# Kernel tuning notes

Hardware: AMD Instinct MI355X
Metric: run time of the kernel (lower is better)

The kernel has to match this reference:

```python
import jax, jax.numpy as jnp
import numpy as np

GRID_SIZE = 5
SPLINE_ORDER = 3
# Extended knot grid over [-1, 1]: grid_size + 2*spline_order + 1 = 12 knots
_H = 2.0 / GRID_SIZE
GRID = (jnp.arange(-SPLINE_ORDER, GRID_SIZE + SPLINE_ORDER + 1, dtype=jnp.float32) * _H - 1.0)


def b_splines(x):
    # x: [N, F] -> bases [N, F, GRID_SIZE + SPLINE_ORDER]
    g = GRID.astype(x.dtype)
    xe = x[..., None]
    bases = ((xe >= g[:-1]) & (xe < g[1:])).astype(x.dtype)
    for k in range(1, SPLINE_ORDER + 1):
        left = (xe - g[: -(k + 1)]) / (g[k:-1] - g[: -(k + 1)]) * bases[..., :-1]
        right = (g[k + 1:] - xe) / (g[k + 1:] - g[1:-k]) * bases[..., 1:]
        bases = left + right
    return bases


def kan_conv(x, base_w, spline_w, spline_scaler):
    # x: [B, Cin, H, W]; 3x3 conv, stride 1, pad 1 -> [B, Cout, H, W]
    B, C, H, W = x.shape
    patches = jax.lax.conv_general_dilated_patches(
        x, (3, 3), (1, 1), [(1, 1), (1, 1)])  # [B, C*9, H, W]
    feat = patches.transpose(0, 2, 3, 1).reshape(B * H * W, C * 9)
    base_out = jax.nn.silu(feat) @ base_w.T  # [N, Cout]
    bas = b_splines(feat)                    # [N, C*9, 8]
    sw = spline_w * spline_scaler[..., None] # standalone spline scale
    spline_out = jnp.einsum('nik,oik->no', bas, sw)
    out = (base_out + spline_out).reshape(B, H, W, -1).transpose(0, 3, 1, 2)
    return out


def upsample2x(x):
    return jnp.repeat(jnp.repeat(x, 2, axis=2), 2, axis=3)


def setup_inputs() -> dict:
    key = jax.random.key(0)
    ks = jax.random.split(key, 16)
    d = {}
    d['x'] = jax.random.normal(ks[0], (64, 100), dtype=jnp.float32)
    d['lin_w'] = jax.random.normal(ks[1], (2048, 100), dtype=jnp.float32) * 0.1
    d['lin_b'] = jax.random.normal(ks[2], (2048,), dtype=jnp.float32) * 0.01
    chans = [(512, 256), (256, 128), (128, 64), (64, 3)]
    i = 3
    for li, (cin, cout) in enumerate(chans, start=1):
        fin = cin * 9
        scale = 1.0 / np.sqrt(fin)
        d[f'bw{li}'] = jax.random.normal(ks[i], (cout, fin), dtype=jnp.float32) * scale; i += 1
        d[f'sw{li}'] = jax.random.normal(ks[i], (cout, fin, GRID_SIZE + SPLINE_ORDER), dtype=jnp.float32) * (0.1 * scale); i += 1
        d[f'ss{li}'] = jax.random.normal(ks[i], (cout, fin), dtype=jnp.float32) * scale + 1.0; i += 1
    return d


def reference(x, lin_w, lin_b, bw1, sw1, ss1, bw2, sw2, ss2, bw3, sw3, ss3, bw4, sw4, ss4):
    h = jax.nn.relu(x @ lin_w.T + lin_b)          # [B, 2048]
    h = h.reshape(-1, 512, 2, 2)                  # Unflatten
    h = upsample2x(h)                             # 4x4
    h = kan_conv(h, bw1, sw1, ss1)                # [B,256,4,4]
    h = upsample2x(h)                             # 8x8
    h = kan_conv(h, bw2, sw2, ss2)                # [B,128,8,8]
    h = upsample2x(h)                             # 16x16
    h = kan_conv(h, bw3, sw3, ss3)                # [B,64,16,16]
    h = upsample2x(h)                             # 32x32
    h = kan_conv(h, bw4, sw4, ss4)                # [B,3,32,32]
    return jnp.tanh(h)
```

## Files before the change

kernel.cpp:

```cpp
#include <hip/hip_runtime.h>
#include <cstdint>
#include <cmath>

#define BATCH 64

typedef __attribute__((ext_vector_type(8))) __bf16 bf16x8;
typedef __attribute__((ext_vector_type(16))) float f32x16;

__device__ __forceinline__ void expand9(float x, float* e) {
  float t = __expf(-x);
  e[0] = __fdividef(x, 1.f + t);
  float b[11];
#pragma unroll
  for (int j = 0; j < 11; ++j) {
    float gj  = 0.4f * (float)j - 2.2f;
    float gj1 = 0.4f * (float)(j + 1) - 2.2f;
    b[j] = (x >= gj && x < gj1) ? 1.f : 0.f;
  }
#pragma unroll
  for (int k = 1; k <= 3; ++k) {
    float inv = 1.f / (0.4f * (float)k);
#pragma unroll
    for (int j = 0; j < 11 - k; ++j) {
      float gj   = 0.4f * (float)j - 2.2f;
      float gjk1 = 0.4f * (float)(j + k + 1) - 2.2f;
      b[j] = ((x - gj) * b[j] + (gjk1 - x) * b[j + 1]) * inv;
    }
  }
#pragma unroll
  for (int v = 0; v < 8; ++v) e[v + 1] = b[v];
}

__device__ __forceinline__ unsigned short f2bf(float x) {
  uint32_t u = __float_as_uint(x);
  uint32_t r = u + 0x7fffu + ((u >> 16) & 1u);
  return (unsigned short)(r >> 16);
}

__device__ __forceinline__ void pack9(const float* e, uint32_t* d) {
  d[0] = (uint32_t)f2bf(e[0]) | ((uint32_t)f2bf(e[1]) << 16);
  d[1] = (uint32_t)f2bf(e[2]) | ((uint32_t)f2bf(e[3]) << 16);
  d[2] = (uint32_t)f2bf(e[4]) | ((uint32_t)f2bf(e[5]) << 16);
  d[3] = (uint32_t)f2bf(e[6]) | ((uint32_t)f2bf(e[7]) << 16);
  d[4] = (uint32_t)f2bf(e[8]);
}

template <int F, int N, int LOGN>
__device__ __forceinline__ void bpack_body(int bid, const float* __restrict__ bw,
                                           const float* __restrict__ sw,
                                           const float* __restrict__ ss,
                                           unsigned short* __restrict__ Bg) {
  int idx = bid * 256 + threadIdx.x;
  int fl = idx & 15;
  int n = (idx >> 4) & (N - 1);
  int kc = idx >> (4 + LOGN);
  int f = kc * 16 + fl;
  size_t src = (size_t)n * F + f;
  float bv = bw[src];
  float sc = ss[src];
  const float4* sp = reinterpret_cast<const float4*>(sw + src * 8);
  float4 s0 = sp[0], s1 = sp[1];
  size_t base = ((size_t)(kc * 9) * N + n) * 16 + fl;
  const size_t vs = (size_t)N * 16;
  Bg[base]          = f2bf(bv);
  Bg[base + vs]     = f2bf(s0.x * sc);
  Bg[base + 2 * vs] = f2bf(s0.y * sc);
  Bg[base + 3 * vs] = f2bf(s0.z * sc);
  Bg[base + 4 * vs] = f2bf(s0.w * sc);
  Bg[base + 5 * vs] = f2bf(s1.x * sc);
  Bg[base + 6 * vs] = f2bf(s1.y * sc);
  Bg[base + 7 * vs] = f2bf(s1.z * sc);
  Bg[base + 8 * vs] = f2bf(s1.w * sc);
}

__device__ __forceinline__ void wnl4_body(int bid, const float* __restrict__ bw,
                                          const float* __restrict__ sw,
                                          const float* __restrict__ ss,
                                          float* __restrict__ Wn) {
  int idx = bid * 256 + threadIdx.x;
  if (idx >= 27648) return;
  int u = idx % 27;
  int o = u % 3, v = u / 3;
  int rest = idx / 27;
  int nb = rest & 3;
  rest >>= 2;
  int pc = rest & 3;
  rest >>= 2;
  int c = rest;
  int PH = pc >> 1, PW = pc & 1;
  int a = nb >> 1, b2 = nb & 1;
  float s = 0.f;
#pragma unroll
  for (int kh = 0; kh < 3; ++kh) {
    if (((kh > PH) ? 1 : 0) != a) continue;
#pragma unroll
    for (int kw = 0; kw < 3; ++kw) {
      if (((kw > PW) ? 1 : 0) != b2) continue;
      int f = c * 9 + kh * 3 + kw;
      float wv = (v == 0)
                     ? bw[o * 576 + f]
                     : sw[((size_t)(o * 576 + f)) * 8 + (v - 1)] * ss[o * 576 + f];
      s += wv;
    }
  }
  Wn[idx] = s;
}

__device__ __forceinline__ void linear_body(int bid, const float* __restrict__ x,
                                            const float* __restrict__ w,
                                            const float* __restrict__ bias,
                                            float* __restrict__ h,
                                            uint32_t* __restrict__ E) {
  int idx = bid * 256 + threadIdx.x;
  int b = idx >> 11, o = idx & 2047;
  const float* xr = x + b * 100;
  const float* wr = w + o * 100;
  float acc = bias[o];
#pragma unroll 4
  for (int k = 0; k < 100; ++k) acc += xr[k] * wr[k];
  float hv = fmaxf(acc, 0.f);
  h[idx] = hv;
  float e[9];
  expand9(hv, e);
  uint32_t d[5];
  pack9(e, d);
  uint4* p = reinterpret_cast<uint4*>(E + (size_t)idx * 8);
  p[0] = make_uint4(d[0], d[1], d[2], d[3]);
  p[1] = make_uint4(d[4], 0u, 0u, 0u);
}

__global__ __launch_bounds__(256) void prep_all(
    const float* __restrict__ x, const float* __restrict__ lin_w,
    const float* __restrict__ lin_b, float* __restrict__ h,
    uint32_t* __restrict__ Eg,
    const float* __restrict__ bw1, const float* __restrict__ sw1,
    const float* __restrict__ ss1, unsigned short* __restrict__ Bg1,
    const float* __restrict__ bw2, const float* __restrict__ sw2,
    const float* __restrict__ ss2, unsigned short* __restrict__ Bg2,
    const float* __restrict__ bw3, const float* __restrict__ sw3,
    const float* __restrict__ ss3, unsigned short* __restrict__ Bg3,
    const float* __restrict__ bw4, const float* __restrict__ sw4,
    const float* __restrict__ ss4, float* __restrict__ wl4) {
  int bid = blockIdx.x;
  if (bid < 4608) { bpack_body<4608, 256, 8>(bid, bw1, sw1, ss1, Bg1); return; }
  bid -= 4608;
  if (bid < 1152) { bpack_body<2304, 128, 7>(bid, bw2, sw2, ss2, Bg2); return; }
  bid -= 1152;
  if (bid < 288) { bpack_body<1152, 64, 6>(bid, bw3, sw3, ss3, Bg3); return; }
  bid -= 288;
  if (bid < 108) { wnl4_body(bid, bw4, sw4, ss4, wl4); return; }
  bid -= 108;
  linear_body(bid, x, lin_w, lin_b, h, Eg);
}

__global__ __launch_bounds__(256) void linear_relu_only(
    const float* __restrict__ x, const float* __restrict__ w,
    const float* __restrict__ bias, float* __restrict__ h) {
  int idx = blockIdx.x * 256 + threadIdx.x;
  int b = idx >> 11, o = idx & 2047;
  const float* xr = x + b * 100;
  const float* wr = w + o * 100;
  float acc = bias[o];
#pragma unroll 4
  for (int k = 0; k < 100; ++k) acc += xr[k] * wr[k];
  h[idx] = fmaxf(acc, 0.f);
}

template <int CIN, int COUT, int HO, int WO, int SK>
__global__ __launch_bounds__(256, 4) void gemm_mfma(
    const uint32_t* __restrict__ E, const unsigned short* __restrict__ Bg,
    float* __restrict__ part) {
  constexpr int F = CIN * 9;
  constexpr int NKC = F / 16;
  constexpr int HI = HO / 2, WI = WO / 2;
  constexpr int M = BATCH * HO * WO;
  constexpr int CPB = NKC / SK;
  static_assert(NKC % SK == 0, "sk");

  __shared__ __align__(16) unsigned short lds[2 * 9216];

  const int t = threadIdx.x;
  const int mbase = blockIdx.x * 64;
  const int nb = blockIdx.y;
  const int kc0 = blockIdx.z * CPB;

  uint32_t ez[5];
  {
    float e0[9];
    expand9(0.f, e0);
    pack9(e0, ez);
  }

  const int lane = t & 63, wv_ = t >> 6;
  const int wm = wv_ >> 1, wn = wv_ & 1;
  const int frow = lane & 31, fkg = lane >> 5;
  const int aoff = ((wm * 32 + frow) * 16 + fkg * 8) * 2;
  const int boff = ((wn * 32 + frow) * 16 + fkg * 8) * 2;

  const int aml = t >> 2, flq = t & 3;
  const int am = mbase + aml;
  const int ab = am / (HO * WO), ahw = am % (HO * WO);
  const int ahh = ahw / WO, aww = ahw % WO;

  f32x16 acc;
#pragma unroll
  for (int i = 0; i < 16; ++i) acc[i] = 0.f;

  for (int ci = 0; ci < CPB; ++ci) {
    const int kc = kc0 + ci;
    __syncthreads();

    {
      uint32_t w0[5], w1[5], w2[5], w3[5];
#define LDTAP(IDX, DST)                                                       \
  {                                                                           \
    int f = kc * 16 + flq * 4 + IDX;                                          \
    int c = f / 9, r = f - 9 * c;                                             \
    int kh = r / 3, kw = r - kh * 3;                                          \
    int hp = ahh + kh - 1, wp = aww + kw - 1;                                 \
    if ((unsigned)hp < (unsigned)HO && (unsigned)wp < (unsigned)WO) {         \
      const uint32_t* ep =                                                    \
          E + (size_t)(((ab * CIN + c) * HI + (hp >> 1)) * WI + (wp >> 1)) *  \
                  8;                                                          \
      uint4 q0 = *reinterpret_cast<const uint4*>(ep);                         \
      DST[0] = q0.x; DST[1] = q0.y; DST[2] = q0.z; DST[3] = q0.w;             \
      DST[4] = ep[4];                                                         \
    } else {                                                                  \
      _Pragma("unroll") for (int v = 0; v < 5; ++v) DST[v] = ez[v];           \
    }                                                                         \
  }
      LDTAP(0, w0)
      LDTAP(1, w1)
      LDTAP(2, w2)
      LDTAP(3, w3)
#undef LDTAP
#define GETV(W, V) (((V)&1) ? ((W)[(V) >> 1] >> 16) : ((W)[(V) >> 1] & 0xffffu))
      char* lb = reinterpret_cast<char*>(lds);
#pragma unroll
      for (int v = 0; v < 9; ++v) {
        uint32_t t0 = GETV(w0, v), t1 = GETV(w1, v);
        uint32_t t2 = GETV(w2, v), t3 = GETV(w3, v);
        uint32_t hi01 = t0 | (t1 << 16);
        uint32_t hi23 = t2 | (t3 << 16);
        *reinterpret_cast<uint2*>(lb + v * 2048 + aml * 32 + flq * 8) =
            make_uint2(hi01, hi23);
      }
#undef GETV
    }

    {
      const unsigned short* bsrc = Bg + (size_t)kc * (9 * COUT * 16);
#define STAGEB(U)                                                             \
  {                                                                           \
    int u = (U);                                                              \
    int v = u >> 7, q = u & 127;                                              \
    int nl = q >> 1, half = q & 1;                                            \
    size_t srcE = (size_t)v * (COUT * 16) + (size_t)(nb * 64 + nl) * 16 +     \
                  half * 8;                                                   \
    int dst = 9216 + v * 1024 + nl * 16 + half * 8;                           \
    *reinterpret_cast<float4*>(&lds[dst]) =                                   \
        *reinterpret_cast<const float4*>(&bsrc[srcE]);                        \
  }
      STAGEB(t)
      STAGEB(256 + t)
      STAGEB(512 + t)
      STAGEB(768 + t)
      if (t < 128) STAGEB(1024 + t)
#undef STAGEB
    }
    __syncthreads();

#pragma unroll
    for (int v = 0; v < 9; ++v) {
      const char* lbc = reinterpret_cast<const char*>(lds);
      bf16x8 ah = *reinterpret_cast<const bf16x8*>(lbc + v * 2048 + aoff);
      bf16x8 bh =
          *reinterpret_cast<const bf16x8*>(lbc + 18432 + v * 2048 + boff);
      acc = __builtin_amdgcn_mfma_f32_32x32x16_bf16(ah, bh, acc, 0, 0, 0);
    }
  }

  float* p = part + (size_t)blockIdx.z * M * COUT;
  const int gn = nb * 64 + wn * 32 + frow;
#pragma unroll
  for (int r = 0; r < 16; ++r) {
    int mlocal = (r & 3) + 8 * (r >> 2) + 4 * fkg;
    int gm = mbase + wm * 32 + mlocal;
    p[(size_t)gm * COUT + gn] = acc[r];
  }
}

template <int COUT, int HO, int WO>
__global__ __launch_bounds__(256) void reduce_pe_pack(
    const float* __restrict__ part, uint32_t* __restrict__ E, int SK) {
  constexpr int M = BATCH * HO * WO;
  int idx = blockIdx.x * 256 + threadIdx.x;
  float s = 0.f;
  for (int k = 0; k < SK; ++k) s += part[(size_t)k * M * COUT + idx];
  int o = idx & (COUT - 1);
  int m = idx / COUT;
  int b = m / (HO * WO);
  int hw = m % (HO * WO);
  int idx2 = ((b * COUT + o) * (HO * WO)) + hw;
  float e[9];
  expand9(s, e);
  uint32_t d[5];
  pack9(e, d);
  uint4* p = reinterpret_cast<uint4*>(E + (size_t)idx2 * 8);
  p[0] = make_uint4(d[0], d[1], d[2], d[3]);
  p[1] = make_uint4(d[4], 0u, 0u, 0u);
}

template <int COUT, int HO, int WO>
__global__ __launch_bounds__(256) void reduce_p(
    const float* __restrict__ part, float* __restrict__ act, int SK) {
  constexpr int M = BATCH * HO * WO;
  int idx = blockIdx.x * 256 + threadIdx.x;
  float s = 0.f;
  for (int k = 0; k < SK; ++k) s += part[(size_t)k * M * COUT + idx];
  int o = idx & (COUT - 1);
  int m = idx / COUT;
  int b = m / (HO * WO);
  int hw = m % (HO * WO);
  act[((b * COUT + o) * (HO * WO)) + hw] = s;
}

template <int PH, int PW>
__device__ void l4v9_wave(const float* __restrict__ eLds,
                          const float* __restrict__ WnB,
                          const float* __restrict__ ez, int lane, int bb,
                          int cs, int qh, float* __restrict__ p4) {
  constexpr int PC = PH * 2 + PW;
  const int j = lane & 15;
  const int i0 = (lane >> 4) << 2;
#pragma unroll 1
  for (int q = 2 * qh; q < 2 * qh + 2; ++q) {
    const int i = i0 + q;
    float acc[3] = {0.f, 0.f, 0.f};
#pragma unroll
    for (int a = 0; a < 2; ++a) {
      const int gi = i + PH - 1 + a;
      const bool vr = (unsigned)gi < 16u;
#pragma unroll
      for (int b2 = 0; b2 < 2; ++b2) {
        const int gj = j + PW - 1 + b2;
        const bool ok = vr && ((unsigned)gj < 16u);
        const int pp = ok ? (gi * 16 + gj) : 0;
        const int nbi = a * 2 + b2;
#pragma unroll
        for (int cl = 0; cl < 2; ++cl) {
          const float* ep = eLds + cl * 2304 + pp * 9;
          float en[9];
#pragma unroll
          for (int v = 0; v < 9; ++v) en[v] = ok ? ep[v] : ez[v];
          const float* wp = WnB + ((cl * 4 + PC) * 4 + nbi) * 27;
#pragma unroll
          for (int v = 0; v < 9; ++v) {
            acc[0] = fmaf(en[v], wp[v * 3 + 0], acc[0]);
            acc[1] = fmaf(en[v], wp[v * 3 + 1], acc[1]);
            acc[2] = fmaf(en[v], wp[v * 3 + 2], acc[2]);
          }
        }
      }
    }
    const int h = (i << 1) + PH, w = (j << 1) + PW;
#pragma unroll
    for (int o = 0; o < 3; ++o)
      p4[(size_t)cs * 196608 + ((bb * 3 + o) << 10) + (h << 5) + w] = acc[o];
  }
}

__global__ __launch_bounds__(256) void kan_l4_v9(
    const float* __restrict__ a3, const float* __restrict__ Wn,
    float* __restrict__ p4) {
  __shared__ float eLds[2 * 256 * 9];
  const int bid = blockIdx.x;
  const int qh = bid & 1, cs = (bid >> 1) & 31, bb = bid >> 6;
  const int t = threadIdx.x;
  float ez[9];
  expand9(0.f, ez);
#pragma unroll
  for (int cl = 0; cl < 2; ++cl) {
    float x = a3[(size_t)(bb * 64 + cs * 2 + cl) * 256 + t];
    float ev[9];
    expand9(x, ev);
#pragma unroll
    for (int v = 0; v < 9; ++v) eLds[(cl * 256 + t) * 9 + v] = ev[v];
  }
  __syncthreads();
  const int wv_ = t >> 6, lane = t & 63;
  const float* WnB = Wn + (size_t)cs * 2 * (4 * 4 * 27);
  if (wv_ == 0)
    l4v9_wave<0, 0>(eLds, WnB, ez, lane, bb, cs, qh, p4);
  else if (wv_ == 1)
    l4v9_wave<0, 1>(eLds, WnB, ez, lane, bb, cs, qh, p4);
  else if (wv_ == 2)
    l4v9_wave<1, 0>(eLds, WnB, ez, lane, bb, cs, qh, p4);
  else
    l4v9_wave<1, 1>(eLds, WnB, ez, lane, bb, cs, qh, p4);
}

__global__ __launch_bounds__(256) void reduce_tanh_l4_32(
    const float* __restrict__ p4, float* __restrict__ out) {
  int i = blockIdx.x * 256 + threadIdx.x;
  float s = 0.f;
#pragma unroll
  for (int k = 0; k < 32; ++k) s += p4[(size_t)k * 196608 + i];
  out[i] = tanhf(s);
}

__global__ __launch_bounds__(256) void reduce_tanh_l4(
    const float* __restrict__ p4, float* __restrict__ out) {
  int i = blockIdx.x * 256 + threadIdx.x;
  float s = p4[i] + p4[i + 196608] + p4[i + 2 * 196608] + p4[i + 3 * 196608];
  out[i] = tanhf(s);
}

template <int CIN, int COUT, int HO, int WO, int BN, int SK>
__global__ __launch_bounds__(256) void kan_gemm(
    const float* __restrict__ in, const float* __restrict__ bw,
    const float* __restrict__ sw, const float* __restrict__ ss,
    float* __restrict__ outp) {
  constexpr int BM = 64, TM = 4, TN = 4, FC = 16;
  constexpr int F = CIN * 9;
  constexpr int HI = HO / 2, WI = WO / 2;
  constexpr int M = BATCH * HO * WO;
  constexpr int FPB = F / SK;

  __shared__ float Ae[FC * 9][BM];

  const int t = threadIdx.x;
  const int mbase = blockIdx.x * BM;
  const int obase = blockIdx.y * BN;
  const int f0 = blockIdx.z * FPB;

  const int cg = t & (BN / TN - 1);
  const int rg = t / (BN / TN);
  const int m0 = rg * TM;
  const int o0 = obase + cg * TN;

  float acc[TM][TN] = {};

  for (int fc = f0; fc < f0 + FPB; fc += FC) {
#pragma unroll
    for (int j = 0; j < BM * FC / 256; ++j) {
      int p = j * 256 + t;
      int ml = p & (BM - 1);
      int df = p >> 6;
      int f = fc + df;
      int c = f / 9;
      int r = f - c * 9;
      int kh = r / 3, kw = r - kh * 3;
      int m = mbase + ml;
      int bb = m / (HO * WO);
      int rem = m % (HO * WO);
      int hh = rem / WO, ww = rem % WO;
      int hp = hh + kh - 1, wp = ww + kw - 1;
      float val = 0.f;
      if (hp >= 0 && hp < HO && wp >= 0 && wp < WO)
        val = in[((bb * CIN + c) * HI + (hp >> 1)) * WI + (wp >> 1)];
      float e[9];
      expand9(val, e);
#pragma unroll
      for (int v = 0; v < 9; ++v) Ae[df * 9 + v][ml] = e[v];
    }
    __syncthreads();

#pragma unroll 2
    for (int df = 0; df < FC; ++df) {
      int f = fc + df;
      float wb[TN], wsv[TN][8];
#pragma unroll
      for (int tn = 0; tn < TN; ++tn) {
        int i = (o0 + tn) * F + f;
        wb[tn] = bw[i];
        float sc = ss[i];
        const float4* sp = reinterpret_cast<const float4*>(sw + (size_t)i * 8);
        float4 s0 = sp[0], s1 = sp[1];
        wsv[tn][0] = s0.x * sc; wsv[tn][1] = s0.y * sc;
        wsv[tn][2] = s0.z * sc; wsv[tn][3] = s0.w * sc;
        wsv[tn][4] = s1.x * sc; wsv[tn][5] = s1.y * sc;
        wsv[tn][6] = s1.z * sc; wsv[tn][7] = s1.w * sc;
      }
      float a[9][TM];
#pragma unroll
      for (int v = 0; v < 9; ++v) {
        float4 q = *reinterpret_cast<const float4*>(&Ae[df * 9 + v][m0]);
        a[v][0] = q.x; a[v][1] = q.y; a[v][2] = q.z; a[v][3] = q.w;
      }
#pragma unroll
      for (int tm = 0; tm < TM; ++tm)
#pragma unroll
        for (int tn = 0; tn < TN; ++tn) acc[tm][tn] += a[0][tm] * wb[tn];
#pragma unroll
      for (int v = 1; v < 9; ++v)
#pragma unroll
        for (int tm = 0; tm < TM; ++tm)
#pragma unroll
          for (int tn = 0; tn < TN; ++tn)
            acc[tm][tn] += a[v][tm] * wsv[tn][v - 1];
    }
    __syncthreads();
  }

  if constexpr (SK > 1) {
    float* p = outp + (size_t)blockIdx.z * M * COUT;
#pragma unroll
    for (int tm = 0; tm < TM; ++tm) {
      int m = mbase + m0 + tm;
#pragma unroll
      for (int tn = 0; tn < TN; ++tn)
        p[(size_t)m * COUT + (o0 + tn)] = acc[tm][tn];
    }
  } else {
#pragma unroll
    for (int tm = 0; tm < TM; ++tm) {
      int m = mbase + m0 + tm;
      int bb = m / (HO * WO);
      int rem = m % (HO * WO);
      int hh = rem / WO, ww = rem % WO;
#pragma unroll
      for (int tn = 0; tn < TN; ++tn) {
        int o = o0 + tn;
        outp[((bb * COUT + o) * HO + hh) * WO + ww] = acc[tm][tn];
      }
    }
  }
}

template <int COUT, int HO, int WO, int SK>
__global__ __launch_bounds__(256) void reduce_partials_old(
    const float* __restrict__ part, float* __restrict__ act) {
  constexpr int M = BATCH * HO * WO;
  int idx = blockIdx.x * 256 + threadIdx.x;
  if (idx >= M * COUT) return;
  float s = 0.f;
#pragma unroll
  for (int k = 0; k < SK; ++k) s += part[(size_t)k * M * COUT + idx];
  int m = idx / COUT, o = idx - (idx / COUT) * COUT;
  int bb = m / (HO * WO);
  int rem = m % (HO * WO);
  int hh = rem / WO, ww = rem % WO;
  act[((bb * COUT + o) * HO + hh) * WO + ww] = s;
}

__global__ __launch_bounds__(256) void kan_l4_split(
    const float* __restrict__ a3, const float* __restrict__ bw,
    const float* __restrict__ sw, const float* __restrict__ ss,
    float* __restrict__ p4) {
  int tid = blockIdx.x * 256 + threadIdx.x;
  int cs = tid >> 16, pix = tid & 65535;
  int b = pix >> 10, rem = pix & 1023, h = rem >> 5, w = rem & 31;
  float acc[3] = {0.f, 0.f, 0.f};
  for (int c = cs * 16; c < cs * 16 + 16; ++c) {
#pragma unroll
    for (int kh = 0; kh < 3; ++kh) {
#pragma unroll
      for (int kw = 0; kw < 3; ++kw) {
        int f = (c * 3 + kh) * 3 + kw;
        int hp = h + kh - 1, wp = w + kw - 1;
        float x = 0.f;
        if ((unsigned)hp < 32u && (unsigned)wp < 32u)
          x = a3[((b * 64 + c) * 16 + (hp >> 1)) * 16 + (wp >> 1)];
        float e[9];
        expand9(x, e);
#pragma unroll
        for (int o = 0; o < 3; ++o) {
          int i = o * 576 + f;
          float d = e[1] * sw[i * 8 + 0];
#pragma unroll
          for (int v = 1; v < 8; ++v) d += e[v + 1] * sw[i * 8 + v];
          acc[o] += e[0] * bw[i] + d * ss[i];
        }
      }
    }
  }
#pragma unroll
  for (int o = 0; o < 3; ++o)
    p4[cs * 196608 + ((b * 3 + o) << 10) + (h << 5) + w] = acc[o];
}

extern "C" void kernel_launch(void* const* d_in, const int* in_sizes, int n_in,
                              void* d_out, int out_size, void* d_ws,
                              size_t ws_size, hipStream_t stream) {
  const float* x     = (const float*)d_in[0];
  const float* lin_w = (const float*)d_in[1];
  const float* lin_b = (const float*)d_in[2];
  const float* bw1 = (const float*)d_in[3];
  const float* sw1 = (const float*)d_in[4];
  const float* ss1 = (const float*)d_in[5];
  const float* bw2 = (const float*)d_in[6];
  const float* sw2 = (const float*)d_in[7];
  const float* ss2 = (const float*)d_in[8];
  const float* bw3 = (const float*)d_in[9];
  const float* sw3 = (const float*)d_in[10];
  const float* ss3 = (const float*)d_in[11];
  const float* bw4 = (const float*)d_in[12];
  const float* sw4 = (const float*)d_in[13];
  const float* ss4 = (const float*)d_in[14];

  float* wsf = (float*)d_ws;
  float* h    = wsf;
  float* a3   = wsf + 131072;
  unsigned short* Bg1 = (unsigned short*)(wsf + 1179648);
  unsigned short* Bg2 = (unsigned short*)(wsf + 6488064);
  unsigned short* Bg3 = (unsigned short*)(wsf + 7815168);
  float* wl4  = wsf + 8146944;
  float* part = wsf + 8174592;
  uint32_t* Eg = (uint32_t*)(wsf + 12368896);
  float* p4   = wsf + 8174592;

  const size_t mainNeed = 16563200ull;

  if (ws_size / 4 >= mainNeed) {
    prep_all<<<6668, 256, 0, stream>>>(
        x, lin_w, lin_b, h, Eg,
        bw1, sw1, ss1, Bg1,
        bw2, sw2, ss2, Bg2,
        bw3, sw3, ss3, Bg3,
        bw4, sw4, ss4, wl4);

    gemm_mfma<512, 256, 4, 4, 16>
        <<<dim3(16, 4, 16), 256, 0, stream>>>(Eg, Bg1, part);
    reduce_pe_pack<256, 4, 4><<<1024, 256, 0, stream>>>(part, Eg, 16);

    gemm_mfma<256, 128, 8, 8, 8>
        <<<dim3(64, 2, 8), 256, 0, stream>>>(Eg, Bg2, part);
    reduce_pe_pack<128, 8, 8><<<2048, 256, 0, stream>>>(part, Eg, 8);

    gemm_mfma<128, 64, 16, 16, 4>
        <<<dim3(256, 1, 4), 256, 0, stream>>>(Eg, Bg3, part);
    reduce_p<64, 16, 16><<<4096, 256, 0, stream>>>(part, a3, 4);

    kan_l4_v9<<<4096, 256, 0, stream>>>(a3, wl4, p4);
    reduce_tanh_l4_32<<<768, 256, 0, stream>>>(p4, (float*)d_out);
  } else {
    float* hF  = wsf;
    float* a1F = hF + 131072;
    float* a2F = a1F + 262144;
    float* a3F = a2F + 524288;
    float* partOld = a3F + 1048576;
    linear_relu_only<<<512, 256, 0, stream>>>(x, lin_w, lin_b, hF);
    kan_gemm<512, 256, 4, 4, 64, 8>
        <<<dim3(16, 4, 8), 256, 0, stream>>>(hF, bw1, sw1, ss1, partOld);
    reduce_partials_old<256, 4, 4, 8><<<1024, 256, 0, stream>>>(partOld, a1F);
    kan_gemm<256, 128, 8, 8, 64, 2>
        <<<dim3(64, 2, 2), 256, 0, stream>>>(a1F, bw2, sw2, ss2, partOld);
    reduce_partials_old<128, 8, 8, 2><<<2048, 256, 0, stream>>>(partOld, a2F);
    kan_gemm<128, 64, 16, 16, 64, 1>
        <<<dim3(256, 1, 1), 256, 0, stream>>>(a2F, bw3, sw3, ss3, a3F);
    kan_l4_split<<<1024, 256, 0, stream>>>(a3F, bw4, sw4, ss4, partOld);
    reduce_tanh_l4<<<768, 256, 0, stream>>>(partOld, (float*)d_out);
  }
}
```

Before: 258.7 us.

## Fold nearest upsample into 2x2 presummed conv weights per output phase

Because each conv input is a nearest-neighbor 2x upsample, the 3x3 taps for each of the four output parity phases collapse onto a 2x2 neighborhood of the low-res input. Weights are presummed per phase, cutting the GEMM K dimension from 9*CIN to 4*CIN, and the output index is remapped to the interleaved high-res position. Layer 2/3 weight prep is moved into a separate launch after the first GEMM. The trade-off is a larger weight workspace (four phase copies) and extra index math in the epilogue. Presumming in fp32 before bf16 rounding also changes rounding slightly.

Measured after the change: 242.4 us. -6.3%, faster.

```diff
diff --git a/kernel.cpp b/kernel.cpp
--- a/kernel.cpp
+++ b/kernel.cpp
@@ -45,32 +45,56 @@
   d[4] = (uint32_t)f2bf(e[8]);
 }
 
-template <int F, int N, int LOGN>
-__device__ __forceinline__ void bpack_body(int bid, const float* __restrict__ bw,
-                                           const float* __restrict__ sw,
-                                           const float* __restrict__ ss,
-                                           unsigned short* __restrict__ Bg) {
+template <int CIN, int N, int LOGN>
+__device__ __forceinline__ void presum_body(int bid,
+                                            const float* __restrict__ bw,
+                                            const float* __restrict__ sw,
+                                            const float* __restrict__ ss,
+                                            unsigned short* __restrict__ Bn) {
+  constexpr int F = CIN * 9;
+  constexpr int KCN = CIN / 4;
   int idx = bid * 256 + threadIdx.x;
-  int fl = idx & 15;
-  int n = (idx >> 4) & (N - 1);
-  int kc = idx >> (4 + LOGN);
-  int f = kc * 16 + fl;
-  size_t src = (size_t)n * F + f;
-  float bv = bw[src];
-  float sc = ss[src];
-  const float4* sp = reinterpret_cast<const float4*>(sw + src * 8);
-  float4 s0 = sp[0], s1 = sp[1];
-  size_t base = ((size_t)(kc * 9) * N + n) * 16 + fl;
-  const size_t vs = (size_t)N * 16;
-  Bg[base]          = f2bf(bv);
-  Bg[base + vs]     = f2bf(s0.x * sc);
-  Bg[base + 2 * vs] = f2bf(s0.y * sc);
-  Bg[base + 3 * vs] = f2bf(s0.z * sc);
-  Bg[base + 4 * vs] = f2bf(s0.w * sc);
-  Bg[base + 5 * vs] = f2bf(s1.x * sc);
-  Bg[base + 6 * vs] = f2bf(s1.y * sc);
-  Bg[base + 7 * vs] = f2bf(s1.z * sc);
-  Bg[base + 8 * vs] = f2bf(s1.w * sc);
+  int n = idx & (N - 1);
+  int c = idx >> LOGN;
+  const float* bwp = bw + (size_t)n * F + c * 9;
+  const float* ssp = ss + (size_t)n * F + c * 9;
+  const float* swp = sw + ((size_t)n * F + c * 9) * 8;
+  float ssv[9];
+#pragma unroll
+  for (int t2 = 0; t2 < 9; ++t2) ssv[t2] = ssp[t2];
+  const int kcn = c >> 2;
+  const int flb = (c & 3) * 4;
+#pragma unroll
+  for (int v = 0; v < 9; ++v) {
+    float tv[9];
+#pragma unroll
+    for (int t2 = 0; t2 < 9; ++t2)
+      tv[t2] = (v == 0) ? bwp[t2] : swp[t2 * 8 + (v - 1)] * ssv[t2];
+#pragma unroll
+    for (int pc = 0; pc < 4; ++pc) {
+      const int PH = pc >> 1, PW = pc & 1;
+      unsigned short u[4];
+#pragma unroll
+      for (int nb = 0; nb < 4; ++nb) {
+        const int a = nb >> 1, b2 = nb & 1;
+        float s = 0.f;
+#pragma unroll
+        for (int kh = 0; kh < 3; ++kh) {
+          if (((kh > PH) ? 1 : 0) != a) continue;
+#pragma unroll
+          for (int kw = 0; kw < 3; ++kw) {
+            if (((kw > PW) ? 1 : 0) != b2) continue;
+            s += tv[kh * 3 + kw];
+          }
+        }
+        u[nb] = f2bf(s);
+      }
+      size_t off = ((((size_t)pc * KCN + kcn) * 9 + v) * N + n) * 16 + flb;
+      *reinterpret_cast<uint2*>(Bn + off) =
+          make_uint2((uint32_t)u[0] | ((uint32_t)u[1] << 16),
+                     (uint32_t)u[2] | ((uint32_t)u[3] << 16));
+    }
+  }
 }
 
 __device__ __forceinline__ void wnl4_body(int bid, const float* __restrict__ bw,
@@ -129,28 +153,31 @@
   p[1] = make_uint4(d[4], 0u, 0u, 0u);
 }
 
-__global__ __launch_bounds__(256) void prep_all(
+__global__ __launch_bounds__(256) void prep_main(
     const float* __restrict__ x, const float* __restrict__ lin_w,
     const float* __restrict__ lin_b, float* __restrict__ h,
     uint32_t* __restrict__ Eg,
     const float* __restrict__ bw1, const float* __restrict__ sw1,
-    const float* __restrict__ ss1, unsigned short* __restrict__ Bg1,
-    const float* __restrict__ bw2, const float* __restrict__ sw2,
-    const float* __restrict__ ss2, unsigned short* __restrict__ Bg2,
-    const float* __restrict__ bw3, const float* __restrict__ sw3,
-    const float* __restrict__ ss3, unsigned short* __restrict__ Bg3,
+    const float* __restrict__ ss1, unsigned short* __restrict__ Bn1,
     const float* __restrict__ bw4, const float* __restrict__ sw4,
     const float* __restrict__ ss4, float* __restrict__ wl4) {
   int bid = blockIdx.x;
-  if (bid < 4608) { bpack_body<4608, 256, 8>(bid, bw1, sw1, ss1, Bg1); return; }
-  bid -= 4608;
-  if (bid < 1152) { bpack_body<2304, 128, 7>(bid, bw2, sw2, ss2, Bg2); return; }
-  bid -= 1152;
-  if (bid < 288) { bpack_body<1152, 64, 6>(bid, bw3, sw3, ss3, Bg3); return; }
-  bid -= 288;
+  if (bid < 512) { presum_body<512, 256, 8>(bid, bw1, sw1, ss1, Bn1); return; }
+  bid -= 512;
   if (bid < 108) { wnl4_body(bid, bw4, sw4, ss4, wl4); return; }
   bid -= 108;
   linear_body(bid, x, lin_w, lin_b, h, Eg);
+}
+
+__global__ __launch_bounds__(256) void prep23(
+    const float* __restrict__ bw2, const float* __restrict__ sw2,
+    const float* __restrict__ ss2, unsigned short* __restrict__ Bn2,
+    const float* __restrict__ bw3, const float* __restrict__ sw3,
+    const float* __restrict__ ss3, unsigned short* __restrict__ Bn3) {
+  int bid = blockIdx.x;
+  if (bid < 128) { presum_body<256, 128, 7>(bid, bw2, sw2, ss2, Bn2); return; }
+  bid -= 128;
+  presum_body<128, 64, 6>(bid, bw3, sw3, ss3, Bn3);
 }
 
 __global__ __launch_bounds__(256) void linear_relu_only(
@@ -168,12 +195,13 @@
 
 template <int CIN, int COUT, int HO, int WO, int SK>
 __global__ __launch_bounds__(256, 4) void gemm_mfma(
-    const uint32_t* __restrict__ E, const unsigned short* __restrict__ Bg,
+    const uint32_t* __restrict__ E, const unsigned short* __restrict__ Bn,
     float* __restrict__ part) {
-  constexpr int F = CIN * 9;
-  constexpr int NKC = F / 16;
-  constexpr int HI = HO / 2, WI = WO / 2;
+  constexpr int HO2 = HO / 2, WO2 = WO / 2;
+  constexpr int NKC = CIN / 4;
   constexpr int M = BATCH * HO * WO;
+  constexpr int MPC = M / 4;
+  constexpr int NB = COUT / 64;
   constexpr int CPB = NKC / SK;
   static_assert(NKC % SK == 0, "sk");
 
@@ -181,8 +209,12 @@
 
   const int t = threadIdx.x;
   const int mbase = blockIdx.x * 64;
-  const int nb = blockIdx.y;
+  const int ybn = blockIdx.y;
+  const int pc = ybn / NB;
+  const int nb = ybn % NB;
+  const int PH = pc >> 1, PW = pc & 1;
   const int kc0 = blockIdx.z * CPB;
+  const unsigned short* BgP = Bn + (size_t)pc * NKC * 9 * COUT * 16;
 
   uint32_t ez[5];
   {
@@ -199,8 +231,9 @@
 
   const int aml = t >> 2, flq = t & 3;
   const int am = mbase + aml;
-  const int ab = am / (HO * WO), ahw = am % (HO * WO);
-  const int ahh = ahw / WO, aww = ahw % WO;
+  const int ab = am / (HO2 * WO2), ahw = am % (HO2 * WO2);
+  const int ihm = ahw / WO2, iwm = ahw % WO2;
+  const int gi0 = ihm + PH - 1, gj0 = iwm + PW - 1;
 
   f32x16 acc;
 #pragma unroll
@@ -211,17 +244,14 @@
     __syncthreads();
 
     {
+      const int cch = kc * 4 + flq;
       uint32_t w0[5], w1[5], w2[5], w3[5];
-#define LDTAP(IDX, DST)                                                       \
+#define LDNB(A, B2, DST)                                                      \
   {                                                                           \
-    int f = kc * 16 + flq * 4 + IDX;                                          \
-    int c = f / 9, r = f - 9 * c;                                             \
-    int kh = r / 3, kw = r - kh * 3;                                          \
-    int hp = ahh + kh - 1, wp = aww + kw - 1;                                 \
-    if ((unsigned)hp < (unsigned)HO && (unsigned)wp < (unsigned)WO) {         \
+    int gi = gi0 + (A), gj = gj0 + (B2);                                      \
+    if ((unsigned)gi < (unsigned)HO2 && (unsigned)gj < (unsigned)WO2) {       \
       const uint32_t* ep =                                                    \
-          E + (size_t)(((ab * CIN + c) * HI + (hp >> 1)) * WI + (wp >> 1)) *  \
-                  8;                                                          \
+          E + (size_t)(((ab * CIN + cch) * HO2 + gi) * WO2 + gj) * 8;         \
       uint4 q0 = *reinterpret_cast<const uint4*>(ep);                         \
       DST[0] = q0.x; DST[1] = q0.y; DST[2] = q0.z; DST[3] = q0.w;             \
       DST[4] = ep[4];                                                         \
@@ -229,11 +259,11 @@
       _Pragma("unroll") for (int v = 0; v < 5; ++v) DST[v] = ez[v];           \
     }                                                                         \
   }
-      LDTAP(0, w0)
-      LDTAP(1, w1)
-      LDTAP(2, w2)
-      LDTAP(3, w3)
-#undef LDTAP
+      LDNB(0, 0, w0)
+      LDNB(0, 1, w1)
+      LDNB(1, 0, w2)
+      LDNB(1, 1, w3)
+#undef LDNB
 #define GETV(W, V) (((V)&1) ? ((W)[(V) >> 1] >> 16) : ((W)[(V) >> 1] & 0xffffu))
       char* lb = reinterpret_cast<char*>(lds);
 #pragma unroll
@@ -249,7 +279,7 @@
     }
 
     {
-      const unsigned short* bsrc = Bg + (size_t)kc * (9 * COUT * 16);
+      const unsigned short* bsrc = BgP + (size_t)kc * (9 * COUT * 16);
 #define STAGEB(U)                                                             \
   {                                                                           \
     int u = (U);                                                              \
@@ -285,7 +315,11 @@
 #pragma unroll
   for (int r = 0; r < 16; ++r) {
     int mlocal = (r & 3) + 8 * (r >> 2) + 4 * fkg;
-    int gm = mbase + wm * 32 + mlocal;
+    int gmp = mbase + wm * 32 + mlocal;
+    int eb = gmp / (HO2 * WO2);
+    int er = gmp % (HO2 * WO2);
+    int eih = er / WO2, eiw = er % WO2;
+    int gm = (eb * HO + 2 * eih + PH) * WO + (2 * eiw + PW);
     p[(size_t)gm * COUT + gn] = acc[r];
   }
 }
@@ -602,34 +636,33 @@
   float* wsf = (float*)d_ws;
   float* h    = wsf;
   float* a3   = wsf + 131072;
-  unsigned short* Bg1 = (unsigned short*)(wsf + 1179648);
-  unsigned short* Bg2 = (unsigned short*)(wsf + 6488064);
-  unsigned short* Bg3 = (unsigned short*)(wsf + 7815168);
-  float* wl4  = wsf + 8146944;
-  float* part = wsf + 8174592;
-  uint32_t* Eg = (uint32_t*)(wsf + 12368896);
-  float* p4   = wsf + 8174592;
-
-  const size_t mainNeed = 16563200ull;
+  unsigned short* Bn1 = (unsigned short*)(wsf + 1179648);
+  unsigned short* Bn2 = (unsigned short*)(wsf + 1179648);
+  unsigned short* Bn3 = (unsigned short*)(wsf + 3538944);
+  float* wl4  = wsf + 10616832;
+  float* part = wsf + 10644480;
+  uint32_t* Eg = (uint32_t*)(wsf + 14838784);
+  float* p4   = wsf + 10644480;
+
+  const size_t mainNeed = 19033088ull;
 
   if (ws_size / 4 >= mainNeed) {
-    prep_all<<<6668, 256, 0, stream>>>(
+    prep_main<<<1132, 256, 0, stream>>>(
         x, lin_w, lin_b, h, Eg,
-        bw1, sw1, ss1, Bg1,
-        bw2, sw2, ss2, Bg2,
-        bw3, sw3, ss3, Bg3,
+        bw1, sw1, ss1, Bn1,
         bw4, sw4, ss4, wl4);
 
     gemm_mfma<512, 256, 4, 4, 16>
-        <<<dim3(16, 4, 16), 256, 0, stream>>>(Eg, Bg1, part);
+        <<<dim3(4, 16, 16), 256, 0, stream>>>(Eg, Bn1, part);
+    prep23<<<160, 256, 0, stream>>>(bw2, sw2, ss2, Bn2, bw3, sw3, ss3, Bn3);
     reduce_pe_pack<256, 4, 4><<<1024, 256, 0, stream>>>(part, Eg, 16);
 
     gemm_mfma<256, 128, 8, 8, 8>
-        <<<dim3(64, 2, 8), 256, 0, stream>>>(Eg, Bg2, part);
+        <<<dim3(16, 8, 8), 256, 0, stream>>>(Eg, Bn2, part);
     reduce_pe_pack<128, 8, 8><<<2048, 256, 0, stream>>>(part, Eg, 8);
 
     gemm_mfma<128, 64, 16, 16, 4>
-        <<<dim3(256, 1, 4), 256, 0, stream>>>(Eg, Bg3, part);
+        <<<dim3(64, 4, 4), 256, 0, stream>>>(Eg, Bn3, part);
     reduce_p<64, 16, 16><<<4096, 256, 0, stream>>>(part, a3, 4);
 
     kan_l4_v9<<<4096, 256, 0, stream>>>(a3, wl4, p4);
```
